# Performance work log

Measured on AMD Instinct MI355X. Metric: run time of the kernel, lower is better.

Reference implementation:

```python
import jax, jax.numpy as jnp
import numpy as np

PC_RANGE = np.array([-75.2, -75.2, -2.0, 75.2, 75.2, 4.0], dtype=np.float32)
NUM_FPS_POINTS = 512
POOL_EXTRA_WIDTH = 1.0
B, M, N = 2, 128, 131072


def setup_inputs() -> dict:
    key = jax.random.key(0)
    k1, k2, k3, k4, k5 = jax.random.split(key, 5)
    # points: (N, 4) [batch_idx, x, y, z] uniform in pc_range
    bidx = jax.random.randint(k1, (N, 1), 0, B).astype(jnp.float32)
    u = jax.random.uniform(k2, (N, 3), dtype=jnp.float32)
    lo = jnp.asarray(PC_RANGE[:3]); hi = jnp.asarray(PC_RANGE[3:])
    xyz = lo + u * (hi - lo)
    points = jnp.concatenate([bidx, xyz], axis=-1)
    # boxes3d: (B, M, 7) [x, y, z, w, l, h, heading] (det3d-style, z at center)
    uc = jax.random.uniform(k3, (B, M, 3), dtype=jnp.float32)
    centers = lo + uc * (hi - lo)
    dims = jnp.asarray([1.8, 4.5, 1.7], jnp.float32) + jax.random.uniform(k4, (B, M, 3), dtype=jnp.float32) * 1.5
    heading = jax.random.uniform(k5, (B, M, 1), dtype=jnp.float32) * (2.0 * np.pi)
    boxes3d = jnp.concatenate([centers, dims, heading], axis=-1)
    return {"points": points, "boxes3d": boxes3d}


def _to_pcdet(b):
    # det3d [x,y,z,w,l,h,r] -> pcdet [x,y,z,dx,dy,dz,heading]: swap w/l, r' = -r - pi/2
    return jnp.concatenate([b[..., 0:3], b[..., 4:5], b[..., 3:4], b[..., 5:6],
                            -(b[..., 6:7] + jnp.pi / 2.0)], axis=-1)


def _pool(points, boxes3d):
    boxes = _to_pcdet(boxes3d)
    # enlarge_box3d: extra_width added on each side
    dims = boxes[..., 3:6] + 2.0 * POOL_EXTRA_WIDTH  # (B, M, 3)
    ctr = boxes[..., 0:3]
    heading = boxes[..., 6]
    pb = points[:, 0].astype(jnp.int32)     # (N,)
    px, py, pz = points[:, 1], points[:, 2], points[:, 3]
    # relative coords, per-box: (B, M, N)
    dx = px[None, None, :] - ctr[..., 0:1]
    dy = py[None, None, :] - ctr[..., 1:2]
    dz = pz[None, None, :] - ctr[..., 2:3]
    c = jnp.cos(heading)[..., None]
    s = jnp.sin(heading)[..., None]
    lx = dx * c + dy * s          # rotate by -heading into box frame
    ly = -dx * s + dy * c
    batch_ok = pb[None, None, :] == jnp.arange(B, dtype=jnp.int32)[:, None, None]
    inside = ((jnp.abs(lx) <= dims[..., 0:1] * 0.5) &
              (jnp.abs(ly) <= dims[..., 1:2] * 0.5) &
              (jnp.abs(dz) <= dims[..., 2:3] * 0.5) & batch_ok)
    count = inside.sum(axis=-1).astype(jnp.int32)                       # (B, M)
    pooled_num = jnp.minimum(count, NUM_FPS_POINTS).astype(jnp.int32)
    # deterministic selection: first NUM_FPS_POINTS in-box point indices (global stacked index)
    score = jnp.where(inside, jnp.arange(N, dtype=jnp.int32), jnp.int32(N))
    idx = jnp.sort(score, axis=-1)[..., :NUM_FPS_POINTS]                # (B, M, 512)
    valid = jnp.arange(NUM_FPS_POINTS, dtype=jnp.int32)[None, None, :] < pooled_num[..., None]
    pooled_idx = jnp.where(valid, idx, 0).astype(jnp.int32)
    return pooled_idx, pooled_num


def reference(points, boxes3d):
    return _pool(points, boxes3d)
```

## Files before the change

### kernel.cpp

```cpp
#include <hip/hip_runtime.h>
#include <math.h>

#define NPTS   131072
#define MBOX   128
#define NBOX   256
#define NFPS   512

#define NTHR   1024
#define NWAVE  16
#define PPW    (NPTS / NWAVE)
#define NGRP   (PPW / 64)
#define DWPB   (NPTS / 32)

__global__ __launch_bounds__(NTHR)
void roi_one(const float* __restrict__ points,
             const float* __restrict__ boxes,
             int* __restrict__ out_idx,
             int* __restrict__ out_num)
{
    const int box  = blockIdx.x;
    const int tid  = threadIdx.x;
    const int lane = tid & 63;
    const int w    = tid >> 6;

    __shared__ unsigned s_bits[DWPB];
    __shared__ int      s_wsum[NWAVE];

    const float4* p4 = (const float4*)points + w * PPW + lane;
    float4 b0[8], b1[8];
    #pragma unroll
    for (int u = 0; u < 8; ++u) b0[u] = p4[u * 64];
    #pragma unroll
    for (int u = 0; u < 8; ++u) b1[u] = p4[(8 + u) * 64];

    const float* bx = boxes + box * 7;
    const float cx = bx[0], cy = bx[1], cz = bx[2];
    const float hx = __fmul_rn(__fadd_rn(bx[4], 2.0f), 0.5f);
    const float hy = __fmul_rn(__fadd_rn(bx[3], 2.0f), 0.5f);
    const float hz = __fmul_rn(__fadd_rn(bx[5], 2.0f), 0.5f);
    const float hp = -__fadd_rn(bx[6], 1.5707963705062866f);
    const float c  = (float)cos((double)hp);
    const float s  = (float)sin((double)hp);
    const float bBf = (float)(box >> 7);

#define ROI_TEST(q, out) do {                                            \
        const float dx_ = __fsub_rn((q).y, cx);                          \
        const float dy_ = __fsub_rn((q).z, cy);                          \
        const float dz_ = __fsub_rn((q).w, cz);                          \
        const float lx_ = __fadd_rn(__fmul_rn(dx_, c), __fmul_rn(dy_, s)); \
        const float ly_ = __fadd_rn(__fmul_rn(-dx_, s), __fmul_rn(dy_, c)); \
        (out) = __ballot(((q).x == bBf) & (fabsf(lx_) <= hx) &           \
                         (fabsf(ly_) <= hy) & (fabsf(dz_) <= hz));       \
    } while (0)

    unsigned long long bal[8];
    #pragma unroll 1
    for (int jo = 0; jo < NGRP; jo += 16) {
        #pragma unroll
        for (int u = 0; u < 8; ++u) ROI_TEST(b0[u], bal[u]);
        if (jo + 16 < NGRP) {
            #pragma unroll
            for (int u = 0; u < 8; ++u) b0[u] = p4[(jo + 16 + u) * 64];
        }
        if (lane == 0) {
            uint4* dst = (uint4*)&s_bits[w * (NGRP * 2) + jo * 2];
            #pragma unroll
            for (int u = 0; u < 4; ++u)
                dst[u] = make_uint4((unsigned)bal[2*u],
                                    (unsigned)(bal[2*u] >> 32),
                                    (unsigned)bal[2*u + 1],
                                    (unsigned)(bal[2*u + 1] >> 32));
        }
        #pragma unroll
        for (int u = 0; u < 8; ++u) ROI_TEST(b1[u], bal[u]);
        if (jo + 24 < NGRP) {
            #pragma unroll
            for (int u = 0; u < 8; ++u) b1[u] = p4[(jo + 24 + u) * 64];
        }
        if (lane == 0) {
            uint4* dst = (uint4*)&s_bits[w * (NGRP * 2) + (jo + 8) * 2];
            #pragma unroll
            for (int u = 0; u < 4; ++u)
                dst[u] = make_uint4((unsigned)bal[2*u],
                                    (unsigned)(bal[2*u] >> 32),
                                    (unsigned)bal[2*u + 1],
                                    (unsigned)(bal[2*u + 1] >> 32));
        }
    }
    __syncthreads();

    const uint4 qv = ((const uint4*)s_bits)[tid];
    unsigned v[4] = {qv.x, qv.y, qv.z, qv.w};
    int cnt = __popc(v[0]) + __popc(v[1]) + __popc(v[2]) + __popc(v[3]);

    int incl = cnt;
    #pragma unroll
    for (int off = 1; off < 64; off <<= 1) {
        const int x = __shfl_up(incl, off, 64);
        if (lane >= off) incl += x;
    }
    if (lane == 63) s_wsum[w] = incl;
    __syncthreads();

    int wpre = 0, total = 0;
    #pragma unroll
    for (int ww = 0; ww < NWAVE; ++ww) {
        const int x = s_wsum[ww];
        if (ww < w) wpre += x;
        total += x;
    }
    int pos = wpre + (incl - cnt);
    const int pn = total < NFPS ? total : NFPS;

    const int obase = box * NFPS;
    if (tid < NFPS && tid >= pn) out_idx[obase + tid] = 0;

    const int pt0 = tid * 128;
    #pragma unroll
    for (int i = 0; i < 4; ++i) {
        unsigned x = v[i];
        while (x) {
            const int bpos = __ffs(x) - 1;
            if (pos < NFPS) out_idx[obase + pos] = pt0 + i * 32 + bpos;
            ++pos;
            x &= x - 1;
        }
    }
    if (tid == 0) out_num[box] = pn;
}

extern "C" void kernel_launch(void* const* d_in, const int* in_sizes, int n_in,
                              void* d_out, int out_size, void* d_ws, size_t ws_size,
                              hipStream_t stream) {
    const float* points = (const float*)d_in[0];
    const float* boxes  = (const float*)d_in[1];
    int* out_idx = (int*)d_out;
    int* out_num = (int*)d_out + NBOX * NFPS;

    roi_one<<<NBOX, NTHR, 0, stream>>>(points, boxes, out_idx, out_num);
}
```

Measured before the change: 26.70 us.

## Stream points through a per-wave LDS ring via global_load_lds

Replaces the register double-buffered point loads with a 7-slot per-wave LDS ring buffer filled by asynchronous global_load_lds (16-byte) transfers, gated by manual s_waitcnt vmcnt. The intent is to free VGPRs and keep several loads in flight without holding 16 float4s per lane. In exchange, each group now makes an LDS round trip, the loop is no longer unrolled, and the ring uses about 114KB of LDS. Correctness depends on the hand-counted vmcnt and on the write slot never overtaking the read slot.

```diff
diff --git a/kernel.cpp b/kernel.cpp
--- a/kernel.cpp
+++ b/kernel.cpp
@@ -11,6 +11,11 @@
 #define PPW    (NPTS / NWAVE)
 #define NGRP   (PPW / 64)
 #define DWPB   (NPTS / 32)
+#define RING   7
+#define MAIN_ITERS (NGRP - 6)
+
+typedef const __attribute__((address_space(1))) void g_void;
+typedef __attribute__((address_space(3))) void l_void;
 
 __global__ __launch_bounds__(NTHR)
 void roi_one(const float* __restrict__ points,
@@ -23,15 +28,9 @@
     const int lane = tid & 63;
     const int w    = tid >> 6;
 
+    __shared__ float4   s_ring[NWAVE][RING][64];
     __shared__ unsigned s_bits[DWPB];
     __shared__ int      s_wsum[NWAVE];
-
-    const float4* p4 = (const float4*)points + w * PPW + lane;
-    float4 b0[8], b1[8];
-    #pragma unroll
-    for (int u = 0; u < 8; ++u) b0[u] = p4[u * 64];
-    #pragma unroll
-    for (int u = 0; u < 8; ++u) b1[u] = p4[(8 + u) * 64];
 
     const float* bx = boxes + box * 7;
     const float cx = bx[0], cy = bx[1], cz = bx[2];
@@ -43,49 +42,54 @@
     const float s  = (float)sin((double)hp);
     const float bBf = (float)(box >> 7);
 
-#define ROI_TEST(q, out) do {                                            \
-        const float dx_ = __fsub_rn((q).y, cx);                          \
-        const float dy_ = __fsub_rn((q).z, cy);                          \
-        const float dz_ = __fsub_rn((q).w, cz);                          \
+    const float4* p4 = (const float4*)points + w * PPW + lane;
+
+    #pragma unroll
+    for (int g = 0; g < 6; ++g)
+        __builtin_amdgcn_global_load_lds((g_void*)(p4 + g * 64),
+                                         (l_void*)&s_ring[w][g][0], 16, 0, 0);
+
+#define ROI_TEST(q, out) do {                                              \
+        const float dx_ = __fsub_rn((q).y, cx);                            \
+        const float dy_ = __fsub_rn((q).z, cy);                            \
+        const float dz_ = __fsub_rn((q).w, cz);                            \
         const float lx_ = __fadd_rn(__fmul_rn(dx_, c), __fmul_rn(dy_, s)); \
         const float ly_ = __fadd_rn(__fmul_rn(-dx_, s), __fmul_rn(dy_, c)); \
-        (out) = __ballot(((q).x == bBf) & (fabsf(lx_) <= hx) &           \
-                         (fabsf(ly_) <= hy) & (fabsf(dz_) <= hz));       \
+        (out) = __ballot(((q).x == bBf) & (fabsf(lx_) <= hx) &             \
+                         (fabsf(ly_) <= hy) & (fabsf(dz_) <= hz));         \
     } while (0)
 
-    unsigned long long bal[8];
+    const float4* gsrc = p4 + 6 * 64;
+    int rslot = 0, wslot = 6;
+
     #pragma unroll 1
-    for (int jo = 0; jo < NGRP; jo += 16) {
-        #pragma unroll
-        for (int u = 0; u < 8; ++u) ROI_TEST(b0[u], bal[u]);
-        if (jo + 16 < NGRP) {
-            #pragma unroll
-            for (int u = 0; u < 8; ++u) b0[u] = p4[(jo + 16 + u) * 64];
-        }
-        if (lane == 0) {
-            uint4* dst = (uint4*)&s_bits[w * (NGRP * 2) + jo * 2];
-            #pragma unroll
-            for (int u = 0; u < 4; ++u)
-                dst[u] = make_uint4((unsigned)bal[2*u],
-                                    (unsigned)(bal[2*u] >> 32),
-                                    (unsigned)bal[2*u + 1],
-                                    (unsigned)(bal[2*u + 1] >> 32));
-        }
-        #pragma unroll
-        for (int u = 0; u < 8; ++u) ROI_TEST(b1[u], bal[u]);
-        if (jo + 24 < NGRP) {
-            #pragma unroll
-            for (int u = 0; u < 8; ++u) b1[u] = p4[(jo + 24 + u) * 64];
-        }
-        if (lane == 0) {
-            uint4* dst = (uint4*)&s_bits[w * (NGRP * 2) + (jo + 8) * 2];
-            #pragma unroll
-            for (int u = 0; u < 4; ++u)
-                dst[u] = make_uint4((unsigned)bal[2*u],
-                                    (unsigned)(bal[2*u] >> 32),
-                                    (unsigned)bal[2*u + 1],
-                                    (unsigned)(bal[2*u + 1] >> 32));
-        }
+    for (int i = 0; i < MAIN_ITERS; ++i) {
+        asm volatile("s_waitcnt vmcnt(5)" ::: "memory");
+        __builtin_amdgcn_sched_barrier(0);
+
+        const float4 q = s_ring[w][rslot][lane];
+        unsigned long long bal;
+        ROI_TEST(q, bal);
+        if (lane == 0)
+            *(unsigned long long*)&s_bits[w * (NGRP * 2) + i * 2] = bal;
+
+        __builtin_amdgcn_global_load_lds((g_void*)gsrc,
+                                         (l_void*)&s_ring[w][wslot][0], 16, 0, 0);
+        gsrc += 64;
+        rslot = (rslot == RING - 1) ? 0 : rslot + 1;
+        wslot = (wslot == RING - 1) ? 0 : wslot + 1;
+    }
+
+    asm volatile("s_waitcnt vmcnt(0)" ::: "memory");
+    __builtin_amdgcn_sched_barrier(0);
+    #pragma unroll 1
+    for (int i = MAIN_ITERS; i < NGRP; ++i) {
+        const float4 q = s_ring[w][rslot][lane];
+        unsigned long long bal;
+        ROI_TEST(q, bal);
+        if (lane == 0)
+            *(unsigned long long*)&s_bits[w * (NGRP * 2) + i * 2] = bal;
+        rslot = (rslot == RING - 1) ? 0 : rslot + 1;
     }
     __syncthreads();
 
```

New measurement: 41.05 us. +53.8%, slower.
